# Optimization experiments

Hardware: AMD Instinct MI355X
Metric: run time of the kernel (lower is better)

Reference implementation:

```python
import jax, jax.numpy as jnp
import numpy as np

TEMP = 0.5
EPS = 1e-8  # torch CosineSimilarity eps


def setup_inputs() -> dict:
    key = jax.random.key(0)
    k1, k2 = jax.random.split(key)
    B, D = 4096, 512
    z_i = jax.random.normal(k1, (B, D), dtype=jnp.float32)
    z_j = jax.random.normal(k2, (B, D), dtype=jnp.float32)
    return {"z_i": z_i, "z_j": z_j}


def reference(z_i, z_j):
    B = z_i.shape[0]
    N = 2 * B
    z = jnp.concatenate([z_i, z_j], axis=0)              # [N, D]
    norm = jnp.maximum(jnp.linalg.norm(z, axis=1, keepdims=True), EPS)
    zn = z / norm                                        # unit rows
    sim = jnp.matmul(zn, zn.T) / TEMP                    # [N, N] cosine sims / temperature
    # positives: sim[i, i+B] for i<B and sim[i+B, i] for i<B
    pos = jnp.concatenate([jnp.diagonal(sim, offset=B), jnp.diagonal(sim, offset=-B)])  # [N]
    # CE over logits [pos, negatives] with label 0 == -pos + logsumexp(row without diagonal)
    diag_mask = jnp.eye(N, dtype=bool)
    sim_masked = jnp.where(diag_mask, -jnp.inf, sim)
    lse = jax.nn.logsumexp(sim_masked, axis=1)           # [N]
    loss = jnp.sum(lse - pos) / N                        # CrossEntropyLoss(reduction='sum') / N
    return loss
```

## Files before the change

kernel.cpp:

```cpp
#include <hip/hip_runtime.h>
#include <stdint.h>

#define NROWS 8192
#define HALF_N 4096
#define DIM 512
#define INV_TEMP 2.0f
#define E2SCALE 2.8853900817779268f
#define LN2 0.6931471805599453f
#define NTILES 2080
#define NXCD 8
#define TPX (NTILES / NXCD)

typedef int i32x8 __attribute__((ext_vector_type(8)));
typedef float f32x16 __attribute__((ext_vector_type(16)));

__device__ __forceinline__ void gload_lds16(const unsigned char* g, unsigned char* l) {
  __builtin_amdgcn_global_load_lds(
      (const __attribute__((address_space(1))) unsigned int*)(uintptr_t)g,
      (__attribute__((address_space(3))) unsigned int*)(uint32_t)(uintptr_t)l,
      16, 0, 0);
}

__global__ void __launch_bounds__(256) k_normalize(const float* __restrict__ zi,
                                                   const float* __restrict__ zj,
                                                   unsigned char* __restrict__ zn,
                                                   float* __restrict__ sumexp) {
  int tid = threadIdx.x;
  int gid = blockIdx.x * 256 + tid;
  if (gid < NROWS) sumexp[gid] = 0.0f;
  int wave = tid >> 6, lane = tid & 63;
  int row = blockIdx.x * 4 + wave;
  const float* src = (row < HALF_N) ? (zi + (size_t)row * DIM)
                                    : (zj + (size_t)(row - HALF_N) * DIM);
  const float4* s4 = (const float4*)src;
  float4 a = s4[lane];
  float4 b = s4[lane + 64];
  float ss = a.x * a.x + a.y * a.y + a.z * a.z + a.w * a.w +
             b.x * b.x + b.y * b.y + b.z * b.z + b.w * b.w;
#pragma unroll
  for (int off = 32; off > 0; off >>= 1) ss += __shfl_xor(ss, off, 64);
  float inv = 1.0f / fmaxf(sqrtf(ss), 1e-8f);
  int w0 = __builtin_amdgcn_cvt_pk_fp8_f32(a.x * inv, a.y * inv, 0, false);
  w0 = __builtin_amdgcn_cvt_pk_fp8_f32(a.z * inv, a.w * inv, w0, true);
  int w1 = __builtin_amdgcn_cvt_pk_fp8_f32(b.x * inv, b.y * inv, 0, false);
  w1 = __builtin_amdgcn_cvt_pk_fp8_f32(b.z * inv, b.w * inv, w1, true);
  unsigned char* dst = zn + (size_t)row * DIM;
  *((int*)(dst + lane * 4)) = w0;
  *((int*)(dst + 256 + lane * 4)) = w1;
}

__global__ void __launch_bounds__(256, 3) k_simsum(const unsigned char* __restrict__ zn,
                                                   float* __restrict__ sumexp,
                                                   float* __restrict__ posv) {
  __shared__ __align__(16) unsigned char As[3][128 * 64];
  __shared__ __align__(16) unsigned char Bs[3][128 * 64];
  int tid = threadIdx.x;
  int wave = tid >> 6, lane = tid & 63;

  int bswz = (blockIdx.x & (NXCD - 1)) * TPX + (blockIdx.x >> 3);
  int idx = bswz;
  int tn = (int)((sqrtf(8.0f * idx + 1.0f) - 1.0f) * 0.5f);
  while (tn * (tn + 1) / 2 > idx) tn--;
  while ((tn + 1) * (tn + 2) / 2 <= idx) tn++;
  int tm = idx - tn * (tn + 1) / 2;
  int rowBase = tm * 128, colBase = tn * 128;
  int wr = (wave >> 1) * 64, wc = (wave & 1) * 64;
  int h = lane >> 5, c32 = lane & 31;

  int rA = wave * 32 + (lane >> 2);
  int chunk = (lane & 3) ^ ((rA >> 1) & 3);
  const unsigned char* gA = zn + (size_t)(rowBase + rA) * DIM + chunk * 16;
  const unsigned char* gB = zn + (size_t)(colBase + rA) * DIM + chunk * 16;

#define STAGE(b)                                          \
  do {                                                    \
    gload_lds16(gA, &As[b][wave * 2048]);                 \
    gload_lds16(gA + 16 * DIM, &As[b][wave * 2048 + 1024]); \
    gload_lds16(gB, &Bs[b][wave * 2048]);                 \
    gload_lds16(gB + 16 * DIM, &Bs[b][wave * 2048 + 1024]); \
    gA += 64; gB += 64;                                   \
  } while (0)

  f32x16 acc[2][2];
#pragma unroll
  for (int i = 0; i < 2; i++)
#pragma unroll
    for (int j = 0; j < 2; j++)
#pragma unroll
      for (int r = 0; r < 16; r++) acc[i][j][r] = 0.f;

  int sg = (c32 >> 1) & 3;
  int p0 = (2 * h) ^ sg, p1 = p0 ^ 1;
  int aIdx[2] = {(wr + c32) * 4, (wr + 32 + c32) * 4};
  int bIdx[2] = {(wc + c32) * 4, (wc + 32 + c32) * 4};

#define COMPUTE(b)                                                                   \
  do {                                                                               \
    const int4* Av = (const int4*)As[b];                                             \
    const int4* Bv = (const int4*)Bs[b];                                             \
    i32x8 af[2], bfr[2];                                                             \
    _Pragma("unroll") for (int i = 0; i < 2; i++) {                                  \
      int4 lo = Av[aIdx[i] + p0], hi = Av[aIdx[i] + p1];                             \
      af[i] = (i32x8){lo.x, lo.y, lo.z, lo.w, hi.x, hi.y, hi.z, hi.w};               \
    }                                                                                \
    _Pragma("unroll") for (int j = 0; j < 2; j++) {                                  \
      int4 lo = Bv[bIdx[j] + p0], hi = Bv[bIdx[j] + p1];                             \
      bfr[j] = (i32x8){lo.x, lo.y, lo.z, lo.w, hi.x, hi.y, hi.z, hi.w};              \
    }                                                                                \
    __builtin_amdgcn_s_setprio(1);                                                   \
    _Pragma("unroll") for (int i = 0; i < 2; i++)                                    \
      _Pragma("unroll") for (int j = 0; j < 2; j++)                                  \
        acc[i][j] = __builtin_amdgcn_mfma_scale_f32_32x32x64_f8f6f4(                 \
            af[i], bfr[j], acc[i][j], 0, 0,                               \
            0, 0x7F, 0, 0x7F);                                     \
    __builtin_amdgcn_s_setprio(0);                                                   \
  } while (0)

#define ASM_VMCNT(n) asm volatile("s_waitcnt vmcnt(" #n ")" ::: "memory")
#define WINDOW(s, vm)                                        \
  do {                                                       \
    ASM_VMCNT(vm);                                           \
    asm volatile("s_waitcnt lgkmcnt(0)" ::: "memory");       \
    __builtin_amdgcn_sched_barrier(0);                       \
    __builtin_amdgcn_s_barrier();                            \
    __builtin_amdgcn_sched_barrier(0);                       \
    if ((s) + 2 < 8) STAGE(((s) + 2) % 3);                   \
    COMPUTE((s) % 3);                                        \
  } while (0)

  STAGE(0);
  STAGE(1);
  WINDOW(0, 4);
  WINDOW(1, 4);
  WINDOW(2, 4);
  WINDOW(3, 4);
  WINDOW(4, 4);
  WINDOW(5, 4);
  WINDOW(6, 4);
  WINDOW(7, 0);

  bool isDiag = (tm == tn);
  bool hasPos = (tn == tm + 32);
  bool diagLane = (wr == wc) && (h == ((c32 >> 2) & 1));
  int rsel = (c32 & 3) | ((c32 >> 3) << 2);

  if (isDiag && diagLane) {
    acc[0][0][rsel] = -1e30f;
    acc[1][1][rsel] = -1e30f;
  }
  if (hasPos && diagLane) {
#pragma unroll
    for (int i = 0; i < 2; i++) {
      float sv = acc[i][i][rsel] * INV_TEMP;
      int gr = rowBase + wr + i * 32 + c32;
      posv[gr] = sv;
      posv[gr + HALF_N] = sv;
    }
  }

  float cp[2] = {0.f, 0.f};
#pragma unroll
  for (int i = 0; i < 2; i++)
#pragma unroll
    for (int r = 0; r < 16; r++) {
      float e0 = __builtin_amdgcn_exp2f(acc[i][0][r] * E2SCALE);
      float e1 = __builtin_amdgcn_exp2f(acc[i][1][r] * E2SCALE);
      cp[0] += e0;
      cp[1] += e1;
      acc[i][0][r] = e0 + e1;
    }

#define RP(t) acc[(t) >> 4][0][(t) & 15]
#pragma unroll
  for (int t = 0; t < 16; t++) {
    float mine = (lane & 16) ? RP(t + 16) : RP(t);
    float oth = __shfl_xor((lane & 16) ? RP(t) : RP(t + 16), 16, 64);
    RP(t) = mine + oth;
  }
#pragma unroll
  for (int t = 0; t < 8; t++) {
    float mine = (lane & 8) ? RP(t + 8) : RP(t);
    float oth = __shfl_xor((lane & 8) ? RP(t) : RP(t + 8), 8, 64);
    RP(t) = mine + oth;
  }
#pragma unroll
  for (int t = 0; t < 4; t++) {
    float mine = (lane & 4) ? RP(t + 4) : RP(t);
    float oth = __shfl_xor((lane & 4) ? RP(t) : RP(t + 4), 4, 64);
    RP(t) = mine + oth;
  }
#pragma unroll
  for (int t = 0; t < 2; t++) {
    float mine = (lane & 2) ? RP(t + 2) : RP(t);
    float oth = __shfl_xor((lane & 2) ? RP(t) : RP(t + 2), 2, 64);
    RP(t) = mine + oth;
  }
  {
    float mine = (lane & 1) ? RP(1) : RP(0);
    float oth = __shfl_xor((lane & 1) ? RP(0) : RP(1), 1, 64);
    RP(0) = mine + oth;
  }
  int myrow = rowBase + wr + 32 * (c32 >> 4) + (c32 & 3) + 8 * ((c32 >> 2) & 3) + 4 * h;
  atomicAdd(&sumexp[myrow], RP(0));
#undef RP

  if (!isDiag) {
    cp[0] += __shfl_xor(cp[0], 32, 64);
    cp[1] += __shfl_xor(cp[1], 32, 64);
    float cv = h ? cp[1] : cp[0];
    atomicAdd(&sumexp[colBase + wc + h * 32 + c32], cv);
  }
#undef STAGE
#undef COMPUTE
#undef WINDOW
#undef ASM_VMCNT
}

__global__ void __launch_bounds__(1024) k_final(const float* __restrict__ sumexp,
                                                const float* __restrict__ posv,
                                                float* __restrict__ out) {
  __shared__ float red[16];
  int tid = threadIdx.x;
  const float4* se4 = (const float4*)sumexp;
  const float4* pv4 = (const float4*)posv;
  float p = 0.f;
#pragma unroll
  for (int c = 0; c < 2; c++) {
    float4 se = se4[tid * 2 + c];
    float4 pv = pv4[tid * 2 + c];
    p += (__builtin_amdgcn_logf(se.x) + __builtin_amdgcn_logf(se.y) +
          __builtin_amdgcn_logf(se.z) + __builtin_amdgcn_logf(se.w)) * LN2 -
         (pv.x + pv.y + pv.z + pv.w);
  }
#pragma unroll
  for (int off = 32; off > 0; off >>= 1) p += __shfl_xor(p, off, 64);
  int wv = tid >> 6, ln = tid & 63;
  if (ln == 0) red[wv] = p;
  __syncthreads();
  if (tid == 0) {
    float t = 0.f;
    for (int w = 0; w < 16; w++) t += red[w];
    out[0] = t / (float)NROWS;
  }
}

extern "C" void kernel_launch(void* const* d_in, const int* in_sizes, int n_in,
                              void* d_out, int out_size, void* d_ws, size_t ws_size,
                              hipStream_t stream) {
  const float* zi = (const float*)d_in[0];
  const float* zj = (const float*)d_in[1];
  unsigned char* zn = (unsigned char*)d_ws;
  float* sumexp = (float*)((char*)d_ws + (size_t)NROWS * DIM);
  float* posv = sumexp + NROWS;
  float* out = (float*)d_out;

  hipLaunchKernelGGL(k_normalize, dim3(2048), dim3(256), 0, stream, zi, zj, zn, sumexp);
  hipLaunchKernelGGL(k_simsum, dim3(NTILES), dim3(256), 0, stream, zn, sumexp, posv);
  hipLaunchKernelGGL(k_final, dim3(1), dim3(1024), 0, stream, sumexp, posv, out);
}
```

Baseline: 91.73 us.

## Enlarge symmetric sim tiles to 256x256 with 8-wave blocks

Tiles of the upper-triangular similarity matrix grow from 128x128 to 256x256, giving 528 tiles instead of 2080. Blocks now use 8 waves, each computing a 128x64 sub-tile with four A fragments. Diagonal masking, positive extraction and the row-sum folds are reworked for the new wave layout. The aim is more operand reuse per LDS byte and fewer atomics and tiles. The cost is more register and LDS pressure, and with 528 blocks the load may spread unevenly across the CUs.

```diff
diff --git a/kernel.cpp b/kernel.cpp
--- a/kernel.cpp
+++ b/kernel.cpp
@@ -7,7 +7,7 @@
 #define INV_TEMP 2.0f
 #define E2SCALE 2.8853900817779268f
 #define LN2 0.6931471805599453f
-#define NTILES 2080
+#define NTILES 528
 #define NXCD 8
 #define TPX (NTILES / NXCD)
 
@@ -49,11 +49,11 @@
   *((int*)(dst + 256 + lane * 4)) = w1;
 }
 
-__global__ void __launch_bounds__(256, 3) k_simsum(const unsigned char* __restrict__ zn,
+__global__ void __launch_bounds__(512, 2) k_simsum(const unsigned char* __restrict__ zn,
                                                    float* __restrict__ sumexp,
                                                    float* __restrict__ posv) {
-  __shared__ __align__(16) unsigned char As[3][128 * 64];
-  __shared__ __align__(16) unsigned char Bs[3][128 * 64];
+  __shared__ __align__(16) unsigned char As[3][256 * 64];
+  __shared__ __align__(16) unsigned char Bs[3][256 * 64];
   int tid = threadIdx.x;
   int wave = tid >> 6, lane = tid & 63;
 
@@ -63,8 +63,8 @@
   while (tn * (tn + 1) / 2 > idx) tn--;
   while ((tn + 1) * (tn + 2) / 2 <= idx) tn++;
   int tm = idx - tn * (tn + 1) / 2;
-  int rowBase = tm * 128, colBase = tn * 128;
-  int wr = (wave >> 1) * 64, wc = (wave & 1) * 64;
+  int rowBase = tm * 256, colBase = tn * 256;
+  int wr = (wave >> 2) * 128, wc = (wave & 3) * 64;
   int h = lane >> 5, c32 = lane & 31;
 
   int rA = wave * 32 + (lane >> 2);
@@ -72,18 +72,18 @@
   const unsigned char* gA = zn + (size_t)(rowBase + rA) * DIM + chunk * 16;
   const unsigned char* gB = zn + (size_t)(colBase + rA) * DIM + chunk * 16;
 
-#define STAGE(b)                                          \
-  do {                                                    \
-    gload_lds16(gA, &As[b][wave * 2048]);                 \
+#define STAGE(b)                                            \
+  do {                                                      \
+    gload_lds16(gA, &As[b][wave * 2048]);                   \
     gload_lds16(gA + 16 * DIM, &As[b][wave * 2048 + 1024]); \
-    gload_lds16(gB, &Bs[b][wave * 2048]);                 \
+    gload_lds16(gB, &Bs[b][wave * 2048]);                   \
     gload_lds16(gB + 16 * DIM, &Bs[b][wave * 2048 + 1024]); \
-    gA += 64; gB += 64;                                   \
-  } while (0)
-
-  f32x16 acc[2][2];
-#pragma unroll
-  for (int i = 0; i < 2; i++)
+    gA += 64; gB += 64;                                     \
+  } while (0)
+
+  f32x16 acc[4][2];
+#pragma unroll
+  for (int i = 0; i < 4; i++)
 #pragma unroll
     for (int j = 0; j < 2; j++)
 #pragma unroll
@@ -91,15 +91,16 @@
 
   int sg = (c32 >> 1) & 3;
   int p0 = (2 * h) ^ sg, p1 = p0 ^ 1;
-  int aIdx[2] = {(wr + c32) * 4, (wr + 32 + c32) * 4};
+  int aIdx[4] = {(wr + c32) * 4, (wr + 32 + c32) * 4,
+                 (wr + 64 + c32) * 4, (wr + 96 + c32) * 4};
   int bIdx[2] = {(wc + c32) * 4, (wc + 32 + c32) * 4};
 
 #define COMPUTE(b)                                                                   \
   do {                                                                               \
     const int4* Av = (const int4*)As[b];                                             \
     const int4* Bv = (const int4*)Bs[b];                                             \
-    i32x8 af[2], bfr[2];                                                             \
-    _Pragma("unroll") for (int i = 0; i < 2; i++) {                                  \
+    i32x8 af[4], bfr[2];                                                             \
+    _Pragma("unroll") for (int i = 0; i < 4; i++) {                                  \
       int4 lo = Av[aIdx[i] + p0], hi = Av[aIdx[i] + p1];                             \
       af[i] = (i32x8){lo.x, lo.y, lo.z, lo.w, hi.x, hi.y, hi.z, hi.w};               \
     }                                                                                \
@@ -108,7 +109,7 @@
       bfr[j] = (i32x8){lo.x, lo.y, lo.z, lo.w, hi.x, hi.y, hi.z, hi.w};              \
     }                                                                                \
     __builtin_amdgcn_s_setprio(1);                                                   \
-    _Pragma("unroll") for (int i = 0; i < 2; i++)                                    \
+    _Pragma("unroll") for (int i = 0; i < 4; i++)                                    \
       _Pragma("unroll") for (int j = 0; j < 2; j++)                                  \
         acc[i][j] = __builtin_amdgcn_mfma_scale_f32_32x32x64_f8f6f4(                 \
             af[i], bfr[j], acc[i][j], 0, 0,                               \
@@ -140,27 +141,34 @@
   WINDOW(7, 0);
 
   bool isDiag = (tm == tn);
-  bool hasPos = (tn == tm + 32);
-  bool diagLane = (wr == wc) && (h == ((c32 >> 2) & 1));
+  bool hasPos = (tn == tm + 16);
+  bool diagLane = (h == ((c32 >> 2) & 1));
   int rsel = (c32 & 3) | ((c32 >> 3) << 2);
-
-  if (isDiag && diagLane) {
-    acc[0][0][rsel] = -1e30f;
-    acc[1][1][rsel] = -1e30f;
-  }
-  if (hasPos && diagLane) {
-#pragma unroll
-    for (int i = 0; i < 2; i++) {
-      float sv = acc[i][i][rsel] * INV_TEMP;
-      int gr = rowBase + wr + i * 32 + c32;
-      posv[gr] = sv;
-      posv[gr + HALF_N] = sv;
+  int dj = 2 * (wave & 3) - 4 * (wave >> 2);
+
+  if (diagLane) {
+    if (isDiag) {
+      if (dj == 0) { acc[0][0][rsel] = -1e30f; acc[1][1][rsel] = -1e30f; }
+      else if (dj == 2) { acc[2][0][rsel] = -1e30f; acc[3][1][rsel] = -1e30f; }
     }
+    if (hasPos) {
+      if (dj == 0) {
+        int gr = rowBase + wr + c32;
+        float s0 = acc[0][0][rsel] * INV_TEMP, s1 = acc[1][1][rsel] * INV_TEMP;
+        posv[gr] = s0; posv[gr + HALF_N] = s0;
+        posv[gr + 32] = s1; posv[gr + 32 + HALF_N] = s1;
+      } else if (dj == 2) {
+        int gr = rowBase + wr + 64 + c32;
+        float s0 = acc[2][0][rsel] * INV_TEMP, s1 = acc[3][1][rsel] * INV_TEMP;
+        posv[gr] = s0; posv[gr + HALF_N] = s0;
+        posv[gr + 32] = s1; posv[gr + 32 + HALF_N] = s1;
+      }
+    }
   }
 
   float cp[2] = {0.f, 0.f};
 #pragma unroll
-  for (int i = 0; i < 2; i++)
+  for (int i = 0; i < 4; i++)
 #pragma unroll
     for (int r = 0; r < 16; r++) {
       float e0 = __builtin_amdgcn_exp2f(acc[i][0][r] * E2SCALE);
@@ -170,39 +178,44 @@
       acc[i][0][r] = e0 + e1;
     }
 
-#define RP(t) acc[(t) >> 4][0][(t) & 15]
-#pragma unroll
-  for (int t = 0; t < 16; t++) {
-    float mine = (lane & 16) ? RP(t + 16) : RP(t);
-    float oth = __shfl_xor((lane & 16) ? RP(t) : RP(t + 16), 16, 64);
-    RP(t) = mine + oth;
-  }
-#pragma unroll
-  for (int t = 0; t < 8; t++) {
-    float mine = (lane & 8) ? RP(t + 8) : RP(t);
-    float oth = __shfl_xor((lane & 8) ? RP(t) : RP(t + 8), 8, 64);
-    RP(t) = mine + oth;
-  }
-#pragma unroll
-  for (int t = 0; t < 4; t++) {
-    float mine = (lane & 4) ? RP(t + 4) : RP(t);
-    float oth = __shfl_xor((lane & 4) ? RP(t) : RP(t + 4), 4, 64);
-    RP(t) = mine + oth;
-  }
-#pragma unroll
-  for (int t = 0; t < 2; t++) {
-    float mine = (lane & 2) ? RP(t + 2) : RP(t);
-    float oth = __shfl_xor((lane & 2) ? RP(t) : RP(t + 2), 2, 64);
-    RP(t) = mine + oth;
-  }
-  {
-    float mine = (lane & 1) ? RP(1) : RP(0);
-    float oth = __shfl_xor((lane & 1) ? RP(0) : RP(1), 1, 64);
-    RP(0) = mine + oth;
-  }
+#define FOLD5(RPX)                                                 \
+  do {                                                             \
+    _Pragma("unroll") for (int t = 0; t < 16; t++) {               \
+      float mine = (lane & 16) ? RPX(t + 16) : RPX(t);             \
+      float oth = __shfl_xor((lane & 16) ? RPX(t) : RPX(t + 16), 16, 64); \
+      RPX(t) = mine + oth;                                         \
+    }                                                              \
+    _Pragma("unroll") for (int t = 0; t < 8; t++) {                \
+      float mine = (lane & 8) ? RPX(t + 8) : RPX(t);               \
+      float oth = __shfl_xor((lane & 8) ? RPX(t) : RPX(t + 8), 8, 64); \
+      RPX(t) = mine + oth;                                         \
+    }                                                              \
+    _Pragma("unroll") for (int t = 0; t < 4; t++) {                \
+      float mine = (lane & 4) ? RPX(t + 4) : RPX(t);               \
+      float oth = __shfl_xor((lane & 4) ? RPX(t) : RPX(t + 4), 4, 64); \
+      RPX(t) = mine + oth;                                         \
+    }                                                              \
+    _Pragma("unroll") for (int t = 0; t < 2; t++) {                \
+      float mine = (lane & 2) ? RPX(t + 2) : RPX(t);               \
+      float oth = __shfl_xor((lane & 2) ? RPX(t) : RPX(t + 2), 2, 64); \
+      RPX(t) = mine + oth;                                         \
+    }                                                              \
+    {                                                              \
+      float mine = (lane & 1) ? RPX(1) : RPX(0);                   \
+      float oth = __shfl_xor((lane & 1) ? RPX(0) : RPX(1), 1, 64); \
+      RPX(0) = mine + oth;                                         \
+    }                                                              \
+  } while (0)
+
+#define RPA(t) acc[(t) >> 4][0][(t) & 15]
+#define RPB(t) acc[2 + ((t) >> 4)][0][(t) & 15]
   int myrow = rowBase + wr + 32 * (c32 >> 4) + (c32 & 3) + 8 * ((c32 >> 2) & 3) + 4 * h;
-  atomicAdd(&sumexp[myrow], RP(0));
-#undef RP
+  FOLD5(RPA);
+  atomicAdd(&sumexp[myrow], RPA(0));
+  FOLD5(RPB);
+  atomicAdd(&sumexp[myrow + 64], RPB(0));
+#undef RPA
+#undef RPB
 
   if (!isDiag) {
     cp[0] += __shfl_xor(cp[0], 32, 64);
@@ -214,6 +227,7 @@
 #undef COMPUTE
 #undef WINDOW
 #undef ASM_VMCNT
+#undef FOLD5
 }
 
 __global__ void __launch_bounds__(1024) k_final(const float* __restrict__ sumexp,
@@ -255,6 +269,6 @@
   float* out = (float*)d_out;
 
   hipLaunchKernelGGL(k_normalize, dim3(2048), dim3(256), 0, stream, zi, zj, zn, sumexp);
-  hipLaunchKernelGGL(k_simsum, dim3(NTILES), dim3(256), 0, stream, zn, sumexp, posv);
+  hipLaunchKernelGGL(k_simsum, dim3(NTILES), dim3(512), 0, stream, zn, sumexp, posv);
   hipLaunchKernelGGL(k_final, dim3(1), dim3(1024), 0, stream, sumexp, posv, out);
 }
```

After: 98.09 us. 1.07x slower.

## Make simsum persistent over 2-3 tiles with cross-tile prefetch pipelining

Applied to the files above, without the earlier changes.

Replaces the one-block-per-tile launch of 2080 blocks with a 768-block grid where each block processes two or three triangular tiles in sequence. The three-stage LDS ring buffer now rotates across tile boundaries, so the first K-chunks of the next tile are prefetched while the current tile's last chunks are computed, and the epilogue is factored into a helper. The aim is to cut launch/tail waves and hide pipeline ramp-up per tile. The cost is a longer per-block critical path, uneven work (2 vs 3 tiles per block), and the epilogue running while the next tile's loads are in flight.

```diff
diff --git a/kernel.cpp b/kernel.cpp
--- a/kernel.cpp
+++ b/kernel.cpp
@@ -7,9 +7,10 @@
 #define INV_TEMP 2.0f
 #define E2SCALE 2.8853900817779268f
 #define LN2 0.6931471805599453f
-#define NTILES 2080
+#define NT128 2080
+#define GRID 768
 #define NXCD 8
-#define TPX (NTILES / NXCD)
+#define TPX (GRID / NXCD)
 
 typedef int i32x8 __attribute__((ext_vector_type(8)));
 typedef float f32x16 __attribute__((ext_vector_type(16)));
@@ -49,36 +50,139 @@
   *((int*)(dst + 256 + lane * 4)) = w1;
 }
 
+__device__ __forceinline__ void epilogue(f32x16 (&acc)[2][2], int tm, int tn,
+                                         int wave, int lane,
+                                         float* __restrict__ sumexp,
+                                         float* __restrict__ posv) {
+  int wr = (wave >> 1) * 64, wc = (wave & 1) * 64;
+  int h = lane >> 5, c32 = lane & 31;
+  int rowBase = tm * 128, colBase = tn * 128;
+  bool isDiag = (tm == tn);
+  bool hasPos = (tn == tm + 32);
+  bool diagLane = (wr == wc) && (h == ((c32 >> 2) & 1));
+  int rsel = (c32 & 3) | ((c32 >> 3) << 2);
+
+  if (isDiag && diagLane) {
+    acc[0][0][rsel] = -1e30f;
+    acc[1][1][rsel] = -1e30f;
+  }
+  if (hasPos && diagLane) {
+#pragma unroll
+    for (int i = 0; i < 2; i++) {
+      float sv = acc[i][i][rsel] * INV_TEMP;
+      int gr = rowBase + wr + i * 32 + c32;
+      posv[gr] = sv;
+      posv[gr + HALF_N] = sv;
+    }
+  }
+
+  float cp[2] = {0.f, 0.f};
+#pragma unroll
+  for (int i = 0; i < 2; i++)
+#pragma unroll
+    for (int r = 0; r < 16; r++) {
+      float e0 = __builtin_amdgcn_exp2f(acc[i][0][r] * E2SCALE);
+      float e1 = __builtin_amdgcn_exp2f(acc[i][1][r] * E2SCALE);
+      cp[0] += e0;
+      cp[1] += e1;
+      acc[i][0][r] = e0 + e1;
+    }
+
+#define RP(t) acc[(t) >> 4][0][(t) & 15]
+#pragma unroll
+  for (int t = 0; t < 16; t++) {
+    float mine = (lane & 16) ? RP(t + 16) : RP(t);
+    float oth = __shfl_xor((lane & 16) ? RP(t) : RP(t + 16), 16, 64);
+    RP(t) = mine + oth;
+  }
+#pragma unroll
+  for (int t = 0; t < 8; t++) {
+    float mine = (lane & 8) ? RP(t + 8) : RP(t);
+    float oth = __shfl_xor((lane & 8) ? RP(t) : RP(t + 8), 8, 64);
+    RP(t) = mine + oth;
+  }
+#pragma unroll
+  for (int t = 0; t < 4; t++) {
+    float mine = (lane & 4) ? RP(t + 4) : RP(t);
+    float oth = __shfl_xor((lane & 4) ? RP(t) : RP(t + 4), 4, 64);
+    RP(t) = mine + oth;
+  }
+#pragma unroll
+  for (int t = 0; t < 2; t++) {
+    float mine = (lane & 2) ? RP(t + 2) : RP(t);
+    float oth = __shfl_xor((lane & 2) ? RP(t) : RP(t + 2), 2, 64);
+    RP(t) = mine + oth;
+  }
+  {
+    float mine = (lane & 1) ? RP(1) : RP(0);
+    float oth = __shfl_xor((lane & 1) ? RP(0) : RP(1), 1, 64);
+    RP(0) = mine + oth;
+  }
+  int myrow = rowBase + wr + 32 * (c32 >> 4) + (c32 & 3) + 8 * ((c32 >> 2) & 3) + 4 * h;
+  atomicAdd(&sumexp[myrow], RP(0));
+#undef RP
+
+  if (!isDiag) {
+    cp[0] += __shfl_xor(cp[0], 32, 64);
+    cp[1] += __shfl_xor(cp[1], 32, 64);
+    float cv = h ? cp[1] : cp[0];
+    atomicAdd(&sumexp[colBase + wc + h * 32 + c32], cv);
+  }
+
+#pragma unroll
+  for (int i = 0; i < 2; i++)
+#pragma unroll
+    for (int j = 0; j < 2; j++)
+#pragma unroll
+      for (int r = 0; r < 16; r++) acc[i][j][r] = 0.f;
+}
+
 __global__ void __launch_bounds__(256, 3) k_simsum(const unsigned char* __restrict__ zn,
                                                    float* __restrict__ sumexp,
                                                    float* __restrict__ posv) {
-  __shared__ __align__(16) unsigned char As[3][128 * 64];
-  __shared__ __align__(16) unsigned char Bs[3][128 * 64];
+  __shared__ __align__(16) unsigned char As[3 * 128 * 64];
+  __shared__ __align__(16) unsigned char Bs[3 * 128 * 64];
   int tid = threadIdx.x;
   int wave = tid >> 6, lane = tid & 63;
 
-  int bswz = (blockIdx.x & (NXCD - 1)) * TPX + (blockIdx.x >> 3);
-  int idx = bswz;
-  int tn = (int)((sqrtf(8.0f * idx + 1.0f) - 1.0f) * 0.5f);
-  while (tn * (tn + 1) / 2 > idx) tn--;
-  while ((tn + 1) * (tn + 2) / 2 <= idx) tn++;
-  int tm = idx - tn * (tn + 1) / 2;
-  int rowBase = tm * 128, colBase = tn * 128;
-  int wr = (wave >> 1) * 64, wc = (wave & 1) * 64;
+  int b = blockIdx.x;
+  int t0 = (b & (NXCD - 1)) * TPX + (b >> 3);
+  int t1 = t0 + GRID;
+  bool has3 = (t0 < NT128 - 2 * GRID);
+  int t2 = t0 + 2 * GRID;
+
+#define DECODE(idx, TM, TN)                                   \
+  do {                                                        \
+    int tn_ = (int)((sqrtf(8.0f * (idx) + 1.0f) - 1.0f) * 0.5f); \
+    while (tn_ * (tn_ + 1) / 2 > (idx)) tn_--;                \
+    while ((tn_ + 1) * (tn_ + 2) / 2 <= (idx)) tn_++;         \
+    TN = tn_; TM = (idx)-tn_ * (tn_ + 1) / 2;                 \
+  } while (0)
+
+  int tm0, tn0, tm1, tn1, tm2 = 0, tn2 = 0;
+  DECODE(t0, tm0, tn0);
+  DECODE(t1, tm1, tn1);
+  if (has3) DECODE(t2, tm2, tn2);
+
   int h = lane >> 5, c32 = lane & 31;
 
   int rA = wave * 32 + (lane >> 2);
   int chunk = (lane & 3) ^ ((rA >> 1) & 3);
-  const unsigned char* gA = zn + (size_t)(rowBase + rA) * DIM + chunk * 16;
-  const unsigned char* gB = zn + (size_t)(colBase + rA) * DIM + chunk * 16;
-
-#define STAGE(b)                                          \
-  do {                                                    \
-    gload_lds16(gA, &As[b][wave * 2048]);                 \
-    gload_lds16(gA + 16 * DIM, &As[b][wave * 2048 + 1024]); \
-    gload_lds16(gB, &Bs[b][wave * 2048]);                 \
-    gload_lds16(gB + 16 * DIM, &Bs[b][wave * 2048 + 1024]); \
-    gA += 64; gB += 64;                                   \
+  const unsigned char* gA = zn + (size_t)(tm0 * 128 + rA) * DIM + chunk * 16;
+  const unsigned char* gB = zn + (size_t)(tn0 * 128 + rA) * DIM + chunk * 16;
+
+  int oC = 0, oM = 8192, oS = 16384;
+#define ROTATE() do { int t_ = oC; oC = oM; oM = oS; oS = t_; } while (0)
+
+#define STAGE_AT(off)                                             \
+  do {                                                            \
+    unsigned char* la = As + (off) + wave * 2048;                 \
+    unsigned char* lb = Bs + (off) + wave * 2048;                 \
+    gload_lds16(gA, la);                                          \
+    gload_lds16(gA + 16 * DIM, la + 1024);                        \
+    gload_lds16(gB, lb);                                          \
+    gload_lds16(gB + 16 * DIM, lb + 1024);                        \
+    gA += 64; gB += 64;                                           \
   } while (0)
 
   f32x16 acc[2][2];
@@ -89,15 +193,16 @@
 #pragma unroll
       for (int r = 0; r < 16; r++) acc[i][j][r] = 0.f;
 
+  int wr = (wave >> 1) * 64, wc = (wave & 1) * 64;
   int sg = (c32 >> 1) & 3;
   int p0 = (2 * h) ^ sg, p1 = p0 ^ 1;
   int aIdx[2] = {(wr + c32) * 4, (wr + 32 + c32) * 4};
   int bIdx[2] = {(wc + c32) * 4, (wc + 32 + c32) * 4};
 
-#define COMPUTE(b)                                                                   \
+#define COMPUTE()                                                                    \
   do {                                                                               \
-    const int4* Av = (const int4*)As[b];                                             \
-    const int4* Bv = (const int4*)Bs[b];                                             \
+    const int4* Av = (const int4*)(As + oC);                                         \
+    const int4* Bv = (const int4*)(Bs + oC);                                         \
     i32x8 af[2], bfr[2];                                                             \
     _Pragma("unroll") for (int i = 0; i < 2; i++) {                                  \
       int4 lo = Av[aIdx[i] + p0], hi = Av[aIdx[i] + p1];                             \
@@ -117,103 +222,60 @@
   } while (0)
 
 #define ASM_VMCNT(n) asm volatile("s_waitcnt vmcnt(" #n ")" ::: "memory")
-#define WINDOW(s, vm)                                        \
+#define SYNC(vm)                                             \
   do {                                                       \
     ASM_VMCNT(vm);                                           \
     asm volatile("s_waitcnt lgkmcnt(0)" ::: "memory");       \
     __builtin_amdgcn_sched_barrier(0);                       \
     __builtin_amdgcn_s_barrier();                            \
     __builtin_amdgcn_sched_barrier(0);                       \
-    if ((s) + 2 < 8) STAGE(((s) + 2) % 3);                   \
-    COMPUTE((s) % 3);                                        \
-  } while (0)
-
-  STAGE(0);
-  STAGE(1);
-  WINDOW(0, 4);
-  WINDOW(1, 4);
-  WINDOW(2, 4);
-  WINDOW(3, 4);
-  WINDOW(4, 4);
-  WINDOW(5, 4);
-  WINDOW(6, 4);
-  WINDOW(7, 0);
-
-  bool isDiag = (tm == tn);
-  bool hasPos = (tn == tm + 32);
-  bool diagLane = (wr == wc) && (h == ((c32 >> 2) & 1));
-  int rsel = (c32 & 3) | ((c32 >> 3) << 2);
-
-  if (isDiag && diagLane) {
-    acc[0][0][rsel] = -1e30f;
-    acc[1][1][rsel] = -1e30f;
-  }
-  if (hasPos && diagLane) {
-#pragma unroll
-    for (int i = 0; i < 2; i++) {
-      float sv = acc[i][i][rsel] * INV_TEMP;
-      int gr = rowBase + wr + i * 32 + c32;
-      posv[gr] = sv;
-      posv[gr + HALF_N] = sv;
-    }
-  }
-
-  float cp[2] = {0.f, 0.f};
-#pragma unroll
-  for (int i = 0; i < 2; i++)
-#pragma unroll
-    for (int r = 0; r < 16; r++) {
-      float e0 = __builtin_amdgcn_exp2f(acc[i][0][r] * E2SCALE);
-      float e1 = __builtin_amdgcn_exp2f(acc[i][1][r] * E2SCALE);
-      cp[0] += e0;
-      cp[1] += e1;
-      acc[i][0][r] = e0 + e1;
-    }
-
-#define RP(t) acc[(t) >> 4][0][(t) & 15]
-#pragma unroll
-  for (int t = 0; t < 16; t++) {
-    float mine = (lane & 16) ? RP(t + 16) : RP(t);
-    float oth = __shfl_xor((lane & 16) ? RP(t) : RP(t + 16), 16, 64);
-    RP(t) = mine + oth;
-  }
-#pragma unroll
-  for (int t = 0; t < 8; t++) {
-    float mine = (lane & 8) ? RP(t + 8) : RP(t);
-    float oth = __shfl_xor((lane & 8) ? RP(t) : RP(t + 8), 8, 64);
-    RP(t) = mine + oth;
-  }
-#pragma unroll
-  for (int t = 0; t < 4; t++) {
-    float mine = (lane & 4) ? RP(t + 4) : RP(t);
-    float oth = __shfl_xor((lane & 4) ? RP(t) : RP(t + 4), 4, 64);
-    RP(t) = mine + oth;
-  }
-#pragma unroll
-  for (int t = 0; t < 2; t++) {
-    float mine = (lane & 2) ? RP(t + 2) : RP(t);
-    float oth = __shfl_xor((lane & 2) ? RP(t) : RP(t + 2), 2, 64);
-    RP(t) = mine + oth;
-  }
-  {
-    float mine = (lane & 1) ? RP(1) : RP(0);
-    float oth = __shfl_xor((lane & 1) ? RP(0) : RP(1), 1, 64);
-    RP(0) = mine + oth;
-  }
-  int myrow = rowBase + wr + 32 * (c32 >> 4) + (c32 & 3) + 8 * ((c32 >> 2) & 3) + 4 * h;
-  atomicAdd(&sumexp[myrow], RP(0));
-#undef RP
-
-  if (!isDiag) {
-    cp[0] += __shfl_xor(cp[0], 32, 64);
-    cp[1] += __shfl_xor(cp[1], 32, 64);
-    float cv = h ? cp[1] : cp[0];
-    atomicAdd(&sumexp[colBase + wc + h * 32 + c32], cv);
-  }
-#undef STAGE
+  } while (0)
+
+#define WINDOW_N(vm)  do { SYNC(vm); STAGE_AT(oS); COMPUTE(); ROTATE(); } while (0)
+#define WINDOW_NOSTAGE(vm) do { SYNC(vm); COMPUTE(); ROTATE(); } while (0)
+
+#define TILE_HEAD(v0, v1)                                       \
+  do { WINDOW_N(v0); WINDOW_N(v1); WINDOW_N(4); WINDOW_N(4);    \
+       WINDOW_N(4); WINDOW_N(4); } while (0)
+#define TILE_TAIL_NEXT(nTm, nTn)                                        \
+  do {                                                                  \
+    SYNC(4);                                                            \
+    gA = zn + (size_t)((nTm) * 128 + rA) * DIM + chunk * 16;            \
+    gB = zn + (size_t)((nTn) * 128 + rA) * DIM + chunk * 16;            \
+    STAGE_AT(oS); COMPUTE(); ROTATE();                                  \
+    SYNC(4); STAGE_AT(oS); COMPUTE(); ROTATE();                         \
+  } while (0)
+#define TILE_TAIL_LAST() do { WINDOW_NOSTAGE(4); WINDOW_NOSTAGE(0); } while (0)
+
+  STAGE_AT(0);
+  STAGE_AT(8192);
+
+  TILE_HEAD(4, 4);
+  TILE_TAIL_NEXT(tm1, tn1);
+  epilogue(acc, tm0, tn0, wave, lane, sumexp, posv);
+
+  TILE_HEAD(6, 6);
+  if (has3) {
+    TILE_TAIL_NEXT(tm2, tn2);
+    epilogue(acc, tm1, tn1, wave, lane, sumexp, posv);
+    TILE_HEAD(6, 6);
+    TILE_TAIL_LAST();
+    epilogue(acc, tm2, tn2, wave, lane, sumexp, posv);
+  } else {
+    TILE_TAIL_LAST();
+    epilogue(acc, tm1, tn1, wave, lane, sumexp, posv);
+  }
+#undef DECODE
+#undef ROTATE
+#undef STAGE_AT
 #undef COMPUTE
-#undef WINDOW
 #undef ASM_VMCNT
+#undef SYNC
+#undef WINDOW_N
+#undef WINDOW_NOSTAGE
+#undef TILE_HEAD
+#undef TILE_TAIL_NEXT
+#undef TILE_TAIL_LAST
 }
 
 __global__ void __launch_bounds__(1024) k_final(const float* __restrict__ sumexp,
@@ -255,6 +317,6 @@
   float* out = (float*)d_out;
 
   hipLaunchKernelGGL(k_normalize, dim3(2048), dim3(256), 0, stream, zi, zj, zn, sumexp);
-  hipLaunchKernelGGL(k_simsum, dim3(NTILES), dim3(256), 0, stream, zn, sumexp, posv);
+  hipLaunchKernelGGL(k_simsum, dim3(GRID), dim3(256), 0, stream, zn, sumexp, posv);
   hipLaunchKernelGGL(k_final, dim3(1), dim3(1024), 0, stream, sumexp, posv, out);
 }
```

Measured after the change: 94.58 us. 3.1% more time.

## Load MFMA operands directly from global memory into registers, dropping LDS staging

Applied to the files above, without the earlier changes.

Replaces the triple-buffered LDS staging (global_load_lds plus barriers) in the similarity kernel with direct per-lane global loads into registers, double-buffered across two register sets. Each wave reads its own A and B rows straight from global/L2, which removes LDS traffic and workgroup barriers. The cost is that the two waves sharing a row block each fetch it separately, raising global/L2 traffic, and register pressure rises under the launch bound of three blocks per CU.

```diff
diff --git a/kernel.cpp b/kernel.cpp
--- a/kernel.cpp
+++ b/kernel.cpp
@@ -13,13 +13,6 @@
 
 typedef int i32x8 __attribute__((ext_vector_type(8)));
 typedef float f32x16 __attribute__((ext_vector_type(16)));
-
-__device__ __forceinline__ void gload_lds16(const unsigned char* g, unsigned char* l) {
-  __builtin_amdgcn_global_load_lds(
-      (const __attribute__((address_space(1))) unsigned int*)(uintptr_t)g,
-      (__attribute__((address_space(3))) unsigned int*)(uint32_t)(uintptr_t)l,
-      16, 0, 0);
-}
 
 __global__ void __launch_bounds__(256) k_normalize(const float* __restrict__ zi,
                                                    const float* __restrict__ zj,
@@ -52,8 +45,6 @@
 __global__ void __launch_bounds__(256, 3) k_simsum(const unsigned char* __restrict__ zn,
                                                    float* __restrict__ sumexp,
                                                    float* __restrict__ posv) {
-  __shared__ __align__(16) unsigned char As[3][128 * 64];
-  __shared__ __align__(16) unsigned char Bs[3][128 * 64];
   int tid = threadIdx.x;
   int wave = tid >> 6, lane = tid & 63;
 
@@ -67,77 +58,65 @@
   int wr = (wave >> 1) * 64, wc = (wave & 1) * 64;
   int h = lane >> 5, c32 = lane & 31;
 
-  int rA = wave * 32 + (lane >> 2);
-  int chunk = (lane & 3) ^ ((rA >> 1) & 3);
-  const unsigned char* gA = zn + (size_t)(rowBase + rA) * DIM + chunk * 16;
-  const unsigned char* gB = zn + (size_t)(colBase + rA) * DIM + chunk * 16;
-
-#define STAGE(b)                                          \
-  do {                                                    \
-    gload_lds16(gA, &As[b][wave * 2048]);                 \
-    gload_lds16(gA + 16 * DIM, &As[b][wave * 2048 + 1024]); \
-    gload_lds16(gB, &Bs[b][wave * 2048]);                 \
-    gload_lds16(gB + 16 * DIM, &Bs[b][wave * 2048 + 1024]); \
-    gA += 64; gB += 64;                                   \
+  const unsigned char* pA0 = zn + (size_t)(rowBase + wr + c32) * DIM + h * 32;
+  const unsigned char* pA1 = pA0 + 32 * DIM;
+  const unsigned char* pB0 = zn + (size_t)(colBase + wc + c32) * DIM + h * 32;
+  const unsigned char* pB1 = pB0 + 32 * DIM;
+
+  f32x16 acc[2][2];
+#pragma unroll
+  for (int i = 0; i < 2; i++)
+#pragma unroll
+    for (int j = 0; j < 2; j++)
+#pragma unroll
+      for (int r = 0; r < 16; r++) acc[i][j][r] = 0.f;
+
+#define PACK8(lo, hi) ((i32x8){lo.x, lo.y, lo.z, lo.w, hi.x, hi.y, hi.z, hi.w})
+#define MF(a, b, c)                                                       \
+  __builtin_amdgcn_mfma_scale_f32_32x32x64_f8f6f4((a), (b), (c), 0, 0,    \
+                                                  0, 0x7F, 0, 0x7F)
+
+  int4 Xa0l, Xa0h, Xa1l, Xa1h, Xb0l, Xb0h, Xb1l, Xb1h;
+  int4 Ya0l, Ya0h, Ya1l, Ya1h, Yb0l, Yb0h, Yb1l, Yb1h;
+
+#define LOADSET(P, koff)                                                  \
+  do {                                                                    \
+    P##a0l = *(const int4*)(pA0 + (koff));                                \
+    P##a0h = *(const int4*)(pA0 + (koff) + 16);                           \
+    P##a1l = *(const int4*)(pA1 + (koff));                                \
+    P##a1h = *(const int4*)(pA1 + (koff) + 16);                           \
+    P##b0l = *(const int4*)(pB0 + (koff));                                \
+    P##b0h = *(const int4*)(pB0 + (koff) + 16);                           \
+    P##b1l = *(const int4*)(pB1 + (koff));                                \
+    P##b1h = *(const int4*)(pB1 + (koff) + 16);                           \
   } while (0)
 
-  f32x16 acc[2][2];
-#pragma unroll
-  for (int i = 0; i < 2; i++)
-#pragma unroll
-    for (int j = 0; j < 2; j++)
-#pragma unroll
-      for (int r = 0; r < 16; r++) acc[i][j][r] = 0.f;
-
-  int sg = (c32 >> 1) & 3;
-  int p0 = (2 * h) ^ sg, p1 = p0 ^ 1;
-  int aIdx[2] = {(wr + c32) * 4, (wr + 32 + c32) * 4};
-  int bIdx[2] = {(wc + c32) * 4, (wc + 32 + c32) * 4};
-
-#define COMPUTE(b)                                                                   \
-  do {                                                                               \
-    const int4* Av = (const int4*)As[b];                                             \
-    const int4* Bv = (const int4*)Bs[b];                                             \
-    i32x8 af[2], bfr[2];                                                             \
-    _Pragma("unroll") for (int i = 0; i < 2; i++) {                                  \
-      int4 lo = Av[aIdx[i] + p0], hi = Av[aIdx[i] + p1];                             \
-      af[i] = (i32x8){lo.x, lo.y, lo.z, lo.w, hi.x, hi.y, hi.z, hi.w};               \
-    }                                                                                \
-    _Pragma("unroll") for (int j = 0; j < 2; j++) {                                  \
-      int4 lo = Bv[bIdx[j] + p0], hi = Bv[bIdx[j] + p1];                             \
-      bfr[j] = (i32x8){lo.x, lo.y, lo.z, lo.w, hi.x, hi.y, hi.z, hi.w};              \
-    }                                                                                \
-    __builtin_amdgcn_s_setprio(1);                                                   \
-    _Pragma("unroll") for (int i = 0; i < 2; i++)                                    \
-      _Pragma("unroll") for (int j = 0; j < 2; j++)                                  \
-        acc[i][j] = __builtin_amdgcn_mfma_scale_f32_32x32x64_f8f6f4(                 \
-            af[i], bfr[j], acc[i][j], 0, 0,                               \
-            0, 0x7F, 0, 0x7F);                                     \
-    __builtin_amdgcn_s_setprio(0);                                                   \
+#define MFMASET(P)                                                        \
+  do {                                                                    \
+    i32x8 af0 = PACK8(P##a0l, P##a0h), af1 = PACK8(P##a1l, P##a1h);       \
+    i32x8 bf0 = PACK8(P##b0l, P##b0h), bf1 = PACK8(P##b1l, P##b1h);       \
+    acc[0][0] = MF(af0, bf0, acc[0][0]);                                  \
+    acc[0][1] = MF(af0, bf1, acc[0][1]);                                  \
+    acc[1][0] = MF(af1, bf0, acc[1][0]);                                  \
+    acc[1][1] = MF(af1, bf1, acc[1][1]);                                  \
   } while (0)
 
-#define ASM_VMCNT(n) asm volatile("s_waitcnt vmcnt(" #n ")" ::: "memory")
-#define WINDOW(s, vm)                                        \
-  do {                                                       \
-    ASM_VMCNT(vm);                                           \
-    asm volatile("s_waitcnt lgkmcnt(0)" ::: "memory");       \
-    __builtin_amdgcn_sched_barrier(0);                       \
-    __builtin_amdgcn_s_barrier();                            \
-    __builtin_amdgcn_sched_barrier(0);                       \
-    if ((s) + 2 < 8) STAGE(((s) + 2) % 3);                   \
-    COMPUTE((s) % 3);                                        \
-  } while (0)
-
-  STAGE(0);
-  STAGE(1);
-  WINDOW(0, 4);
-  WINDOW(1, 4);
-  WINDOW(2, 4);
-  WINDOW(3, 4);
-  WINDOW(4, 4);
-  WINDOW(5, 4);
-  WINDOW(6, 4);
-  WINDOW(7, 0);
+  LOADSET(X, 0);
+  LOADSET(Y, 64);
+  MFMASET(X);
+  LOADSET(X, 128);
+  MFMASET(Y);
+  LOADSET(Y, 192);
+  MFMASET(X);
+  LOADSET(X, 256);
+  MFMASET(Y);
+  LOADSET(Y, 320);
+  MFMASET(X);
+  LOADSET(X, 384);
+  MFMASET(Y);
+  LOADSET(Y, 448);
+  MFMASET(X);
+  MFMASET(Y);
 
   bool isDiag = (tm == tn);
   bool hasPos = (tn == tm + 32);
@@ -210,10 +189,10 @@
     float cv = h ? cp[1] : cp[0];
     atomicAdd(&sumexp[colBase + wc + h * 32 + c32], cv);
   }
-#undef STAGE
-#undef COMPUTE
-#undef WINDOW
-#undef ASM_VMCNT
+#undef PACK8
+#undef MF
+#undef LOADSET
+#undef MFMASET
 }
 
 __global__ void __launch_bounds__(1024) k_final(const float* __restrict__ sumexp,
```

After: 134.5 us. +46.6%, slower.
